# Kernel optimization log

Hardware: AMD Instinct MI355X
Metric: run time of the kernel (lower is better)

The kernel has to match this reference:

```python
import math
import jax, jax.numpy as jnp
import numpy as np

BATCH, DEPTH = 16, 12
N_NODES = 2 ** DEPTH - 1  # 4095, heap layout: children of i are 2i+1, 2i+2
IN_F, OUT_F, STATE_F = 512, 512, 256


def setup_inputs() -> dict:
    key = jax.random.key(0)
    ks = jax.random.split(key, 10)
    x_batch = jax.random.normal(ks[0], (BATCH, N_NODES, IN_F), dtype=jnp.float32)
    idx_batch = jnp.arange(BATCH, dtype=jnp.int32)
    W_in = jax.random.normal(ks[1], (IN_F, IN_F), dtype=jnp.float32) / math.sqrt(IN_F)
    b_in = jnp.zeros((IN_F,), dtype=jnp.float32)
    u1 = jax.random.uniform(ks[2], (STATE_F,), dtype=jnp.float32)
    u2 = jax.random.uniform(ks[3], (STATE_F,), dtype=jnp.float32)
    nu_log = jnp.log(-0.5 * jnp.log(u1 + 1e-6))
    theta_log = jnp.log(2.0 * math.pi * u2)
    lam_mod = jnp.exp(-jnp.exp(nu_log))
    gamma_log = jnp.log(jnp.sqrt(1.0 - jnp.square(lam_mod)))
    B_re = jax.random.normal(ks[4], (STATE_F, IN_F), dtype=jnp.float32) / math.sqrt(2 * IN_F)
    B_im = jax.random.normal(ks[5], (STATE_F, IN_F), dtype=jnp.float32) / math.sqrt(2 * IN_F)
    C_re = jax.random.normal(ks[6], (OUT_F, STATE_F), dtype=jnp.float32) / math.sqrt(STATE_F)
    C_im = jax.random.normal(ks[7], (OUT_F, STATE_F), dtype=jnp.float32) / math.sqrt(STATE_F)
    return dict(x_batch=x_batch, idx_batch=idx_batch, W_in=W_in, b_in=b_in,
                nu_log=nu_log, theta_log=theta_log, gamma_log=gamma_log,
                B_re=B_re, B_im=B_im, C_re=C_re, C_im=C_im)


def reference(x_batch, idx_batch, W_in, b_in, nu_log, theta_log, gamma_log,
              B_re, B_im, C_re, C_im):
    bsz, n_nodes, _ = x_batch.shape
    depth = int(round(math.log2(n_nodes + 1)))
    S = B_re.shape[0]

    # LRU constants (complex lambda kept as (re, im) pair)
    lam_mod = jnp.exp(-jnp.exp(nu_log))           # [S]
    th = jnp.exp(theta_log)
    lr, li = lam_mod * jnp.cos(th), lam_mod * jnp.sin(th)
    gamma = jnp.exp(gamma_log)                    # [S]

    proj = x_batch @ W_in.T + b_in                # [B, N, IN]
    # complex input term (proj is real): proj @ B^T
    in_re = jnp.einsum('bni,si->bns', proj, B_re) # [B, N, S]
    in_im = jnp.einsum('bni,si->bns', proj, B_im)

    h_re = jnp.zeros((bsz, n_nodes, S), dtype=proj.dtype)
    h_im = jnp.zeros((bsz, n_nodes, S), dtype=proj.dtype)

    # process levels bottom-up; level d nodes occupy [2^d-1, 2^{d+1}-1)
    for d in range(depth - 1, -1, -1):
        a, b = 2 ** d - 1, 2 ** (d + 1) - 1
        n = b - a
        if d == depth - 1:  # leaves: left/right = -1 -> zero child state
            cr = jnp.zeros((bsz, n, S), dtype=proj.dtype)
            ci = jnp.zeros((bsz, n, S), dtype=proj.dtype)
        else:
            # children of nodes [a, b) are the contiguous block [2a+1, 2b+1)
            cr = h_re[:, 2 * a + 1:2 * b + 1].reshape(bsz, n, 2, S).sum(axis=2)
            ci = h_im[:, 2 * a + 1:2 * b + 1].reshape(bsz, n, 2, S).sum(axis=2)
        hr = lr * cr - li * ci + gamma * in_re[:, a:b]
        hi = lr * ci + li * cr + gamma * in_im[:, a:b]
        h_re = h_re.at[:, a:b].set(hr)
        h_im = h_im.at[:, a:b].set(hi)

    # y = Re(h @ C^T), computed once on final states (same math as per-level scatter)
    outputs = jnp.einsum('bns,os->bno', h_re, C_re) - jnp.einsum('bns,os->bno', h_im, C_im)
    return outputs
```

## Files before the change

### kernel.cpp

```cpp
#include <hip/hip_runtime.h>


#define ROWS 65520
#define KDIM 512

typedef __attribute__((ext_vector_type(8))) short bf16x8;
typedef __attribute__((ext_vector_type(4))) float f32x4;

__device__ __forceinline__ unsigned short f2bf(float f) {
    unsigned int u = __float_as_uint(f);
    unsigned int r = (u + 0x7FFFu + ((u >> 16) & 1u)) >> 16;
    return (unsigned short)r;
}
__device__ __forceinline__ float b2f(unsigned short h) {
    return __uint_as_float(((unsigned int)h) << 16);
}
__device__ __forceinline__ float b2f_lo(unsigned int p) {
    return __uint_as_float(p << 16);
}
__device__ __forceinline__ float b2f_hi(unsigned int p) {
    return __uint_as_float(p & 0xFFFF0000u);
}

#define PC_BASE   1024
#define PB_BASE   2048
#define CVT_BASE  2176
#define CVT_BLKS  2048
#define PREP_GRID 4224
#define CVT_N4    8386560

__global__ __launch_bounds__(256) void prep_all(const float* __restrict__ x,
                                                unsigned short* __restrict__ x16,
                                                const float* __restrict__ W,
                                                const float* __restrict__ Bre,
                                                const float* __restrict__ Bim,
                                                const float* __restrict__ gamma_log,
                                                unsigned short* __restrict__ M16,
                                                const float* __restrict__ bin,
                                                float* __restrict__ biasc,
                                                const float* __restrict__ Cre,
                                                const float* __restrict__ Cim,
                                                unsigned short* __restrict__ C16) {
    __shared__ float Bs[16][17];
    __shared__ float Ws[16][17];
    const int blk = blockIdx.x;
    const int t = threadIdx.x;

    if (blk < PC_BASE) {
        const int bx = blk & 31;
        const int by = blk >> 5;
        const int tx = t & 15;
        const int ty = t >> 4;
        const int j  = bx * 16 + tx;
        const int cc = by * 16 + ty;
        const float* Bsel = (cc < 256) ? (Bre + (size_t)cc * 512)
                                       : (Bim + (size_t)(cc - 256) * 512);
        float acc = 0.f;
        for (int kt = 0; kt < 512; kt += 16) {
            Bs[ty][tx] = Bsel[kt + tx];
            Ws[ty][tx] = W[(size_t)(kt + ty) * 512 + j];
            __syncthreads();
#pragma unroll
            for (int k = 0; k < 16; ++k) acc += Bs[ty][k] * Ws[k][tx];
            __syncthreads();
        }
        float g = expf(gamma_log[cc & 255]);
        M16[(size_t)cc * 512 + j] = f2bf(acc * g);
    } else if (blk < PB_BASE) {
        int idx = (blk - PC_BASE) * 256 + t;
        int o = idx >> 9;
        int s = idx & 511;
        float v = (s < 256) ? Cre[(size_t)o * 256 + s] : -Cim[(size_t)o * 256 + (s - 256)];
        C16[idx] = f2bf(v);
    } else if (blk < CVT_BASE) {
        const int c = (blk - PB_BASE) * 4 + (t >> 6);
        const int lane = t & 63;
        const float* Bsel = (c < 256) ? (Bre + (size_t)c * 512)
                                      : (Bim + (size_t)(c - 256) * 512);
        float acc = 0.f;
#pragma unroll
        for (int i = lane; i < 512; i += 64) acc += bin[i] * Bsel[i];
#pragma unroll
        for (int off = 32; off > 0; off >>= 1) acc += __shfl_down(acc, off, 64);
        if (lane == 0) biasc[c] = acc * expf(gamma_log[c & 255]);
    } else {
        int i = (blk - CVT_BASE) * 256 + t;
#pragma unroll 4
        for (; i < CVT_N4; i += CVT_BLKS * 256) {
            float4 v = ((const float4*)x)[i];
            ushort4 o;
            o.x = f2bf(v.x); o.y = f2bf(v.y); o.z = f2bf(v.z); o.w = f2bf(v.w);
            ((ushort4*)x16)[i] = o;
        }
    }
}

template <bool OUT_BF16>
__global__ __launch_bounds__(256) void gemm_mfma(const unsigned short* __restrict__ A,
                                                 const unsigned short* __restrict__ Bm,
                                                 const float* __restrict__ bias,
                                                 void* __restrict__ Cout,
                                                 int Mrows) {
    __shared__ __align__(16) unsigned short As[2][128 * 64];
    __shared__ __align__(16) unsigned short Bs[2][128 * 64];
    const int t = threadIdx.x;
    const int lane = t & 63;
    const int w = t >> 6;
    const int wr = (w >> 1) * 64;
    const int wc = (w & 1) * 64;
    const int bid = blockIdx.x;
    const int xcd = bid & 7;
    const int lid = bid >> 3;
    const int rowblk = xcd * 64 + (lid >> 2);
    const int colblk = lid & 3;
    const int row0 = rowblk * 128;
    const int col0 = colblk * 128;
    const int kt0  = (rowblk & 7) * 64;

    f32x4 acc[4][4] = {};

    const unsigned short* gaB[4];
    const unsigned short* gbB[4];
    int ldsoff[4];
#pragma unroll
    for (int q = 0; q < 4; ++q) {
        int c_   = q * 256 + t;
        int row_ = c_ >> 3;
        int kc_  = c_ & 7;
        int kg_  = kc_ ^ (row_ & 7);
        int ar_  = row0 + row_; if (ar_ >= Mrows) ar_ = Mrows - 1;
        gaB[q] = A + (size_t)ar_ * KDIM + kg_ * 8;
        gbB[q] = Bm + (size_t)(col0 + row_) * KDIM + kg_ * 8;
        ldsoff[q] = c_ * 8;
    }

#define STAGE(pb, itv)                                                         \
    do {                                                                       \
        const int kt_ = (kt0 + (itv) * 64) & 511;                              \
        _Pragma("unroll")                                                      \
        for (int q = 0; q < 4; ++q) {                                          \
            __builtin_amdgcn_global_load_lds(                                  \
                (const __attribute__((address_space(1))) unsigned int*)(gaB[q] + kt_),\
                (__attribute__((address_space(3))) unsigned int*)(&As[pb][ldsoff[q]]),\
                16, 0, 0);                                                     \
            __builtin_amdgcn_global_load_lds(                                  \
                (const __attribute__((address_space(1))) unsigned int*)(gbB[q] + kt_),\
                (__attribute__((address_space(3))) unsigned int*)(&Bs[pb][ldsoff[q]]),\
                16, 0, 0);                                                     \
        }                                                                      \
    } while (0)

    STAGE(0, 0);
    __syncthreads();

    int cur = 0;
    for (int it = 0; it < 8; ++it) {
        if (it < 7) STAGE(cur ^ 1, it + 1);
        __builtin_amdgcn_s_setprio(1);
#pragma unroll
        for (int kk = 0; kk < 64; kk += 32) {
            const int kgc = kk >> 3;
            bf16x8 af[4], bfr[4];
#pragma unroll
            for (int i = 0; i < 4; ++i) {
                int row = wr + i * 16 + (lane & 15);
                int kca = (kgc + (lane >> 4)) ^ (row & 7);
                af[i] = *(const bf16x8*)(&As[cur][row * 64 + kca * 8]);
                int colr = wc + i * 16 + (lane & 15);
                int kcb = (kgc + (lane >> 4)) ^ (colr & 7);
                bfr[i] = *(const bf16x8*)(&Bs[cur][colr * 64 + kcb * 8]);
            }
#pragma unroll
            for (int i = 0; i < 4; ++i)
#pragma unroll
                for (int j = 0; j < 4; ++j)
                    acc[i][j] = __builtin_amdgcn_mfma_f32_16x16x32_bf16(
                        af[i], bfr[j], acc[i][j], 0, 0, 0);
        }
        __builtin_amdgcn_s_setprio(0);
        __syncthreads();
        cur ^= 1;
    }
#undef STAGE

    const int cq = lane >> 4;
    const int cl = lane & 15;
#pragma unroll
    for (int i = 0; i < 4; ++i) {
#pragma unroll
        for (int j = 0; j < 4; ++j) {
#pragma unroll
            for (int r = 0; r < 4; ++r) {
                int grow = row0 + wr + i * 16 + cq * 4 + r;
                int gcol = col0 + wc + j * 16 + cl;
                if (grow < Mrows) {
                    float v = acc[i][j][r];
                    if (bias) v += bias[gcol];
                    if (OUT_BF16)
                        ((unsigned short*)Cout)[(size_t)grow * 512 + gcol] = f2bf(v);
                    else
                        ((float*)Cout)[(size_t)grow * 512 + gcol] = v;
                }
            }
        }
    }
}

template <int E>
__global__ __launch_bounds__(256) void tree_up2(unsigned short* __restrict__ buf,
                                                const float* __restrict__ nu_log,
                                                const float* __restrict__ theta_log,
                                                int root_base, int nroots) {
    const int b = blockIdx.x;
    const int h = threadIdx.x >> 7;
    const int j2 = (threadIdx.x & 127) * 2;
    const int rr = blockIdx.y * 2 + h;
    if (rr >= nroots) return;
    const int rs = root_base + rr;
    constexpr int LEAVES = 1 << E;
    constexpr int NODES = LEAVES - 1;

    float lr0, li0, lr1, li1;
    { const float lam = expf(-expf(nu_log[j2]));     const float th = expf(theta_log[j2]);
      lr0 = lam * cosf(th); li0 = lam * sinf(th); }
    { const float lam = expf(-expf(nu_log[j2 + 1])); const float th = expf(theta_log[j2 + 1]);
      lr1 = lam * cosf(th); li1 = lam * sinf(th); }
    const size_t base = (size_t)b * 4095;

    unsigned int pr[LEAVES], pi[LEAVES];
    const int nbL = ((rs + 1) << E) - 1;
#pragma unroll
    for (int i = 0; i < LEAVES; ++i) {
        const size_t r = (base + nbL + i) * 512;
        pr[i] = *(const unsigned int*)(buf + r + j2);
        pi[i] = *(const unsigned int*)(buf + r + 256 + j2);
    }
    unsigned int qr[NODES], qi[NODES];
#pragma unroll
    for (int e = E - 1; e >= 0; --e) {
#pragma unroll
        for (int i = 0; i < (1 << e); ++i) {
            const int idx = LEAVES - (2 << e) + i;
            const size_t r = (base + (((rs + 1) << e) - 1) + i) * 512;
            qr[idx] = *(const unsigned int*)(buf + r + j2);
            qi[idx] = *(const unsigned int*)(buf + r + 256 + j2);
        }
    }
    __builtin_amdgcn_sched_barrier(0);

    float vr0[LEAVES], vi0[LEAVES], vr1[LEAVES], vi1[LEAVES];
#pragma unroll
    for (int i = 0; i < LEAVES; ++i) {
        vr0[i] = b2f_lo(pr[i]); vr1[i] = b2f_hi(pr[i]);
        vi0[i] = b2f_lo(pi[i]); vi1[i] = b2f_hi(pi[i]);
    }
#pragma unroll
    for (int e = E - 1; e >= 0; --e) {
#pragma unroll
        for (int i = 0; i < (1 << e); ++i) {
            const int idx = LEAVES - (2 << e) + i;
            const float cr0 = vr0[2 * i] + vr0[2 * i + 1];
            const float ci0 = vi0[2 * i] + vi0[2 * i + 1];
            const float cr1 = vr1[2 * i] + vr1[2 * i + 1];
            const float ci1 = vi1[2 * i] + vi1[2 * i + 1];
            const float hr0 = lr0 * cr0 - li0 * ci0 + b2f_lo(qr[idx]);
            const float hi0 = lr0 * ci0 + li0 * cr0 + b2f_lo(qi[idx]);
            const float hr1 = lr1 * cr1 - li1 * ci1 + b2f_hi(qr[idx]);
            const float hi1 = lr1 * ci1 + li1 * cr1 + b2f_hi(qi[idx]);
            const size_t r = (base + (((rs + 1) << e) - 1) + i) * 512;
            *(unsigned int*)(buf + r + j2) =
                (unsigned int)f2bf(hr0) | ((unsigned int)f2bf(hr1) << 16);
            *(unsigned int*)(buf + r + 256 + j2) =
                (unsigned int)f2bf(hi0) | ((unsigned int)f2bf(hi1) << 16);
            vr0[i] = hr0; vi0[i] = hi0; vr1[i] = hr1; vi1[i] = hi1;
        }
    }
}

extern "C" void kernel_launch(void* const* d_in, const int* in_sizes, int n_in,
                              void* d_out, int out_size, void* d_ws, size_t ws_size,
                              hipStream_t stream) {
    const float* x         = (const float*)d_in[0];
    const float* W_in      = (const float*)d_in[2];
    const float* b_in      = (const float*)d_in[3];
    const float* nu_log    = (const float*)d_in[4];
    const float* theta_log = (const float*)d_in[5];
    const float* gamma_log = (const float*)d_in[6];
    const float* B_re      = (const float*)d_in[7];
    const float* B_im      = (const float*)d_in[8];
    const float* C_re      = (const float*)d_in[9];
    const float* C_im      = (const float*)d_in[10];
    float* out = (float*)d_out;

    char* ws = (char*)d_ws;
    const size_t HB = (size_t)ROWS * 512 * 2;
    unsigned short* x16   = (unsigned short*)ws;
    unsigned short* hb16  = (unsigned short*)(ws + HB);
    unsigned short* M16   = (unsigned short*)(ws + 2 * HB);
    unsigned short* C16   = (unsigned short*)(ws + 2 * HB + 512 * 512 * 2);
    float*          biasc = (float*)(ws + 2 * HB + 2 * 512 * 512 * 2);

    prep_all<<<PREP_GRID, 256, 0, stream>>>(x, x16, W_in, B_re, B_im, gamma_log,
                                            M16, b_in, biasc, C_re, C_im, C16);

    gemm_mfma<true><<<2048, 256, 0, stream>>>(x16, M16, biasc, hb16, ROWS);

    tree_up2<4><<<dim3(16, 64), 256, 0, stream>>>(hb16, nu_log, theta_log, 127, 128);
    tree_up2<4><<<dim3(16, 4),  256, 0, stream>>>(hb16, nu_log, theta_log, 7, 8);
    tree_up2<3><<<dim3(16, 1),  256, 0, stream>>>(hb16, nu_log, theta_log, 0, 1);

    gemm_mfma<false><<<2048, 256, 0, stream>>>(hb16, C16, nullptr, out, ROWS);
}
```

Before: 399.9 us.

## Replace double-buffered K=64 stages with 4-deep K=32 pipeline and fragment-ordered LDS

Moves the GEMM main loop from two 64-wide K buffers with a full __syncthreads per step to a four-slot ring of 32-wide K tiles, keeping three tiles in flight. Each step uses explicit vmcnt waits and a single barrier. LDS is rearranged so each lane's MFMA fragment sits in a contiguous slot, which removes the XOR swizzle and per-load index math. The per-block K rotation offset is dropped. The risks are more barriers per unit of work, and bank conflicts or unchanged occupancy from the new layout.

Measured after the change: 459.5 us. +14.9%, slower.

```diff
diff --git a/kernel.cpp b/kernel.cpp
--- a/kernel.cpp
+++ b/kernel.cpp
@@ -101,8 +101,8 @@
                                                  const float* __restrict__ bias,
                                                  void* __restrict__ Cout,
                                                  int Mrows) {
-    __shared__ __align__(16) unsigned short As[2][128 * 64];
-    __shared__ __align__(16) unsigned short Bs[2][128 * 64];
+    __shared__ __align__(16) unsigned short As[4 * 4096];
+    __shared__ __align__(16) unsigned short Bs[4 * 4096];
     const int t = threadIdx.x;
     const int lane = t & 63;
     const int w = t >> 6;
@@ -115,72 +115,92 @@
     const int colblk = lid & 3;
     const int row0 = rowblk * 128;
     const int col0 = colblk * 128;
-    const int kt0  = (rowblk & 7) * 64;
 
     f32x4 acc[4][4] = {};
 
-    const unsigned short* gaB[4];
-    const unsigned short* gbB[4];
-    int ldsoff[4];
-#pragma unroll
-    for (int q = 0; q < 4; ++q) {
-        int c_   = q * 256 + t;
-        int row_ = c_ >> 3;
-        int kc_  = c_ & 7;
-        int kg_  = kc_ ^ (row_ & 7);
-        int ar_  = row0 + row_; if (ar_ >= Mrows) ar_ = Mrows - 1;
-        gaB[q] = A + (size_t)ar_ * KDIM + kg_ * 8;
-        gbB[q] = Bm + (size_t)(col0 + row_) * KDIM + kg_ * 8;
-        ldsoff[q] = c_ * 8;
-    }
-
-#define STAGE(pb, itv)                                                         \
+    const unsigned short* gaB[2];
+    const unsigned short* gbB[2];
+    int sl[2];
+#pragma unroll
+    for (int q = 0; q < 2; ++q) {
+        const int s   = q * 256 + t;
+        const int row = ((s >> 5) << 3) + (s & 7);
+        const int kc  = (s >> 3) & 3;
+        int ar = row0 + row; if (ar >= Mrows) ar = Mrows - 1;
+        gaB[q] = A + (size_t)ar * KDIM + kc * 8;
+        gbB[q] = Bm + (size_t)(col0 + row) * KDIM + kc * 8;
+        sl[q] = s;
+    }
+
+    const int l15 = lane & 15;
+    const int aslot = ((wr >> 3) + (l15 >> 3)) * 32 + ((lane >> 4) << 3) + (lane & 7);
+    const int bslot = ((wc >> 3) + (l15 >> 3)) * 32 + ((lane >> 4) << 3) + (lane & 7);
+
+#define STAGE(PB, IT)                                                          \
     do {                                                                       \
-        const int kt_ = (kt0 + (itv) * 64) & 511;                              \
         _Pragma("unroll")                                                      \
-        for (int q = 0; q < 4; ++q) {                                          \
+        for (int q = 0; q < 2; ++q) {                                          \
             __builtin_amdgcn_global_load_lds(                                  \
-                (const __attribute__((address_space(1))) unsigned int*)(gaB[q] + kt_),\
-                (__attribute__((address_space(3))) unsigned int*)(&As[pb][ldsoff[q]]),\
+                (const __attribute__((address_space(1))) unsigned int*)(gaB[q] + (IT) * 32), \
+                (__attribute__((address_space(3))) unsigned int*)(As + (PB) * 4096 + sl[q] * 8), \
                 16, 0, 0);                                                     \
             __builtin_amdgcn_global_load_lds(                                  \
-                (const __attribute__((address_space(1))) unsigned int*)(gbB[q] + kt_),\
-                (__attribute__((address_space(3))) unsigned int*)(&Bs[pb][ldsoff[q]]),\
+                (const __attribute__((address_space(1))) unsigned int*)(gbB[q] + (IT) * 32), \
+                (__attribute__((address_space(3))) unsigned int*)(Bs + (PB) * 4096 + sl[q] * 8), \
                 16, 0, 0);                                                     \
         }                                                                      \
     } while (0)
 
+#define COMPUTE(PB)                                                            \
+    do {                                                                       \
+        bf16x8 af[4], bfr[4];                                                  \
+        _Pragma("unroll")                                                      \
+        for (int i = 0; i < 4; ++i)                                            \
+            af[i] = *(const bf16x8*)(As + (PB) * 4096 + (aslot + i * 64) * 8); \
+        _Pragma("unroll")                                                      \
+        for (int j = 0; j < 4; ++j)                                            \
+            bfr[j] = *(const bf16x8*)(Bs + (PB) * 4096 + (bslot + j * 64) * 8);\
+        _Pragma("unroll")                                                      \
+        for (int i = 0; i < 4; ++i)                                            \
+            _Pragma("unroll")                                                  \
+            for (int j = 0; j < 4; ++j)                                        \
+                acc[i][j] = __builtin_amdgcn_mfma_f32_16x16x32_bf16(           \
+                    af[i], bfr[j], acc[i][j], 0, 0, 0);                        \
+    } while (0)
+
+#define PIPE_ITER(IT, WAITN, DOSTAGE)                                          \
+    do {                                                                       \
+        asm volatile("s_waitcnt vmcnt(" #WAITN ")" ::: "memory");              \
+        __builtin_amdgcn_s_barrier();                                          \
+        if (DOSTAGE) STAGE((IT + 3) & 3, IT + 3);                              \
+        __builtin_amdgcn_s_setprio(1);                                         \
+        COMPUTE((IT) & 3);                                                     \
+        __builtin_amdgcn_s_setprio(0);                                         \
+    } while (0)
+
     STAGE(0, 0);
-    __syncthreads();
-
-    int cur = 0;
-    for (int it = 0; it < 8; ++it) {
-        if (it < 7) STAGE(cur ^ 1, it + 1);
-        __builtin_amdgcn_s_setprio(1);
-#pragma unroll
-        for (int kk = 0; kk < 64; kk += 32) {
-            const int kgc = kk >> 3;
-            bf16x8 af[4], bfr[4];
-#pragma unroll
-            for (int i = 0; i < 4; ++i) {
-                int row = wr + i * 16 + (lane & 15);
-                int kca = (kgc + (lane >> 4)) ^ (row & 7);
-                af[i] = *(const bf16x8*)(&As[cur][row * 64 + kca * 8]);
-                int colr = wc + i * 16 + (lane & 15);
-                int kcb = (kgc + (lane >> 4)) ^ (colr & 7);
-                bfr[i] = *(const bf16x8*)(&Bs[cur][colr * 64 + kcb * 8]);
-            }
-#pragma unroll
-            for (int i = 0; i < 4; ++i)
-#pragma unroll
-                for (int j = 0; j < 4; ++j)
-                    acc[i][j] = __builtin_amdgcn_mfma_f32_16x16x32_bf16(
-                        af[i], bfr[j], acc[i][j], 0, 0, 0);
-        }
-        __builtin_amdgcn_s_setprio(0);
-        __syncthreads();
-        cur ^= 1;
-    }
+    STAGE(1, 1);
+    STAGE(2, 2);
+
+    PIPE_ITER(0, 8, true);
+    PIPE_ITER(1, 8, true);
+    PIPE_ITER(2, 8, true);
+    PIPE_ITER(3, 8, true);
+    PIPE_ITER(4, 8, true);
+    PIPE_ITER(5, 8, true);
+    PIPE_ITER(6, 8, true);
+    PIPE_ITER(7, 8, true);
+    PIPE_ITER(8, 8, true);
+    PIPE_ITER(9, 8, true);
+    PIPE_ITER(10, 8, true);
+    PIPE_ITER(11, 8, true);
+    PIPE_ITER(12, 8, true);
+    PIPE_ITER(13, 8, false);
+    PIPE_ITER(14, 4, false);
+    PIPE_ITER(15, 0, false);
+
+#undef PIPE_ITER
+#undef COMPUTE
 #undef STAGE
 
     const int cq = lane >> 4;
```

## Make GEMM persistent over four row tiles with cross-tile prefetch

Applied to the files above, without the earlier changes.

Each GEMM workgroup now walks four consecutive 128-row tiles instead of one, and the grid shrinks from 2048 to 512 blocks. The A tile for the next row block is prefetched into LDS during the last k-step of the current tile, so the pipeline stays full across tiles and per-block launch and prologue costs are amortised. The trade-off is fewer resident blocks (512 across 256 CUs) and an epilogue store that is not overlapped with the next tile's compute, which can reduce latency hiding and load balance.

New measurement: 398.4 us. About the same (-0.4%).

```diff
diff --git a/kernel.cpp b/kernel.cpp
--- a/kernel.cpp
+++ b/kernel.cpp
@@ -108,102 +108,126 @@
     const int w = t >> 6;
     const int wr = (w >> 1) * 64;
     const int wc = (w & 1) * 64;
-    const int bid = blockIdx.x;
-    const int xcd = bid & 7;
-    const int lid = bid >> 3;
-    const int rowblk = xcd * 64 + (lid >> 2);
-    const int colblk = lid & 3;
-    const int row0 = rowblk * 128;
+    const int p = blockIdx.x;
+    const int xcd = p & 7;
+    const int q = p >> 3;
+    const int colblk = q & 3;
+    const int rg = q >> 2;
     const int col0 = colblk * 128;
-    const int kt0  = (rowblk & 7) * 64;
-
-    f32x4 acc[4][4] = {};
-
-    const unsigned short* gaB[4];
+
+    int arow[4], akoff[4], ldsoff[4];
     const unsigned short* gbB[4];
-    int ldsoff[4];
-#pragma unroll
-    for (int q = 0; q < 4; ++q) {
-        int c_   = q * 256 + t;
+#pragma unroll
+    for (int qq = 0; qq < 4; ++qq) {
+        int c_   = qq * 256 + t;
         int row_ = c_ >> 3;
         int kc_  = c_ & 7;
         int kg_  = kc_ ^ (row_ & 7);
-        int ar_  = row0 + row_; if (ar_ >= Mrows) ar_ = Mrows - 1;
-        gaB[q] = A + (size_t)ar_ * KDIM + kg_ * 8;
-        gbB[q] = Bm + (size_t)(col0 + row_) * KDIM + kg_ * 8;
-        ldsoff[q] = c_ * 8;
-    }
-
-#define STAGE(pb, itv)                                                         \
+        arow[qq]  = row_;
+        akoff[qq] = kg_ * 8;
+        ldsoff[qq] = c_ * 8;
+        gbB[qq] = Bm + (size_t)(col0 + row_) * KDIM + kg_ * 8;
+    }
+    const unsigned short* gaB[4];
+
+#define SET_TILE_A(ROW0)                                                       \
     do {                                                                       \
-        const int kt_ = (kt0 + (itv) * 64) & 511;                              \
         _Pragma("unroll")                                                      \
-        for (int q = 0; q < 4; ++q) {                                          \
+        for (int qq = 0; qq < 4; ++qq) {                                       \
+            int ar_ = (ROW0) + arow[qq]; if (ar_ >= Mrows) ar_ = Mrows - 1;    \
+            gaB[qq] = A + (size_t)ar_ * KDIM + akoff[qq];                      \
+        }                                                                      \
+    } while (0)
+
+#define STAGE(pb, KT)                                                          \
+    do {                                                                       \
+        _Pragma("unroll")                                                      \
+        for (int qq = 0; qq < 4; ++qq) {                                       \
             __builtin_amdgcn_global_load_lds(                                  \
-                (const __attribute__((address_space(1))) unsigned int*)(gaB[q] + kt_),\
-                (__attribute__((address_space(3))) unsigned int*)(&As[pb][ldsoff[q]]),\
+                (const __attribute__((address_space(1))) unsigned int*)(gaB[qq] + (KT)), \
+                (__attribute__((address_space(3))) unsigned int*)(&As[pb][ldsoff[qq]]), \
                 16, 0, 0);                                                     \
             __builtin_amdgcn_global_load_lds(                                  \
-                (const __attribute__((address_space(1))) unsigned int*)(gbB[q] + kt_),\
-                (__attribute__((address_space(3))) unsigned int*)(&Bs[pb][ldsoff[q]]),\
+                (const __attribute__((address_space(1))) unsigned int*)(gbB[qq] + (KT)), \
+                (__attribute__((address_space(3))) unsigned int*)(&Bs[pb][ldsoff[qq]]), \
                 16, 0, 0);                                                     \
         }                                                                      \
     } while (0)
 
-    STAGE(0, 0);
+    f32x4 acc[4][4] = {};
+
+    int rowblk = xcd * 64 + rg * 4;
+    int row0 = rowblk * 128;
+    int kt0 = (rowblk & 7) * 64;
+    SET_TILE_A(row0);
+    STAGE(0, kt0);
     __syncthreads();
 
     int cur = 0;
-    for (int it = 0; it < 8; ++it) {
-        if (it < 7) STAGE(cur ^ 1, it + 1);
-        __builtin_amdgcn_s_setprio(1);
-#pragma unroll
-        for (int kk = 0; kk < 64; kk += 32) {
-            const int kgc = kk >> 3;
-            bf16x8 af[4], bfr[4];
-#pragma unroll
-            for (int i = 0; i < 4; ++i) {
-                int row = wr + i * 16 + (lane & 15);
-                int kca = (kgc + (lane >> 4)) ^ (row & 7);
-                af[i] = *(const bf16x8*)(&As[cur][row * 64 + kca * 8]);
-                int colr = wc + i * 16 + (lane & 15);
-                int kcb = (kgc + (lane >> 4)) ^ (colr & 7);
-                bfr[i] = *(const bf16x8*)(&Bs[cur][colr * 64 + kcb * 8]);
+    for (int j = 0; j < 4; ++j) {
+        for (int it = 0; it < 8; ++it) {
+            if (it < 7) {
+                STAGE(cur ^ 1, (kt0 + (it + 1) * 64) & 511);
+            } else if (j < 3) {
+                const int nrowblk = rowblk + 1;
+                SET_TILE_A(nrowblk * 128);
+                STAGE(cur ^ 1, (nrowblk & 7) * 64);
             }
-#pragma unroll
-            for (int i = 0; i < 4; ++i)
-#pragma unroll
-                for (int j = 0; j < 4; ++j)
-                    acc[i][j] = __builtin_amdgcn_mfma_f32_16x16x32_bf16(
-                        af[i], bfr[j], acc[i][j], 0, 0, 0);
-        }
-        __builtin_amdgcn_s_setprio(0);
-        __syncthreads();
-        cur ^= 1;
-    }
-#undef STAGE
-
-    const int cq = lane >> 4;
-    const int cl = lane & 15;
-#pragma unroll
-    for (int i = 0; i < 4; ++i) {
-#pragma unroll
-        for (int j = 0; j < 4; ++j) {
-#pragma unroll
-            for (int r = 0; r < 4; ++r) {
-                int grow = row0 + wr + i * 16 + cq * 4 + r;
-                int gcol = col0 + wc + j * 16 + cl;
-                if (grow < Mrows) {
-                    float v = acc[i][j][r];
-                    if (bias) v += bias[gcol];
-                    if (OUT_BF16)
-                        ((unsigned short*)Cout)[(size_t)grow * 512 + gcol] = f2bf(v);
-                    else
-                        ((float*)Cout)[(size_t)grow * 512 + gcol] = v;
+            __builtin_amdgcn_s_setprio(1);
+#pragma unroll
+            for (int kk = 0; kk < 64; kk += 32) {
+                const int kgc = kk >> 3;
+                bf16x8 af[4], bfr[4];
+#pragma unroll
+                for (int i = 0; i < 4; ++i) {
+                    int row = wr + i * 16 + (lane & 15);
+                    int kca = (kgc + (lane >> 4)) ^ (row & 7);
+                    af[i] = *(const bf16x8*)(&As[cur][row * 64 + kca * 8]);
+                    int colr = wc + i * 16 + (lane & 15);
+                    int kcb = (kgc + (lane >> 4)) ^ (colr & 7);
+                    bfr[i] = *(const bf16x8*)(&Bs[cur][colr * 64 + kcb * 8]);
+                }
+#pragma unroll
+                for (int i = 0; i < 4; ++i)
+#pragma unroll
+                    for (int jj = 0; jj < 4; ++jj)
+                        acc[i][jj] = __builtin_amdgcn_mfma_f32_16x16x32_bf16(
+                            af[i], bfr[jj], acc[i][jj], 0, 0, 0);
+            }
+            __builtin_amdgcn_s_setprio(0);
+            __syncthreads();
+            cur ^= 1;
+        }
+
+        const int cq = lane >> 4;
+        const int cl = lane & 15;
+#pragma unroll
+        for (int i = 0; i < 4; ++i) {
+#pragma unroll
+            for (int jj = 0; jj < 4; ++jj) {
+#pragma unroll
+                for (int r = 0; r < 4; ++r) {
+                    int grow = row0 + wr + i * 16 + cq * 4 + r;
+                    int gcol = col0 + wc + jj * 16 + cl;
+                    if (grow < Mrows) {
+                        float v = acc[i][jj][r];
+                        if (bias) v += bias[gcol];
+                        if (OUT_BF16)
+                            ((unsigned short*)Cout)[(size_t)grow * 512 + gcol] = f2bf(v);
+                        else
+                            ((float*)Cout)[(size_t)grow * 512 + gcol] = v;
+                    }
+                    acc[i][jj][r] = 0.f;
                 }
             }
         }
-    }
+
+        rowblk += 1;
+        row0 = rowblk * 128;
+        kt0 = (rowblk & 7) * 64;
+    }
+#undef STAGE
+#undef SET_TILE_A
 }
 
 template <int E>
@@ -303,11 +327,11 @@
     prep_all<<<PREP_GRID, 256, 0, stream>>>(x, x16, W_in, B_re, B_im, gamma_log,
                                             M16, b_in, biasc, C_re, C_im, C16);
 
-    gemm_mfma<true><<<2048, 256, 0, stream>>>(x16, M16, biasc, hb16, ROWS);
+    gemm_mfma<true><<<512, 256, 0, stream>>>(x16, M16, biasc, hb16, ROWS);
 
     tree_up2<4><<<dim3(16, 64), 256, 0, stream>>>(hb16, nu_log, theta_log, 127, 128);
     tree_up2<4><<<dim3(16, 4),  256, 0, stream>>>(hb16, nu_log, theta_log, 7, 8);
     tree_up2<3><<<dim3(16, 1),  256, 0, stream>>>(hb16, nu_log, theta_log, 0, 1);
 
-    gemm_mfma<false><<<2048, 256, 0, stream>>>(hb16, C16, nullptr, out, ROWS);
-}
+    gemm_mfma<false><<<512, 256, 0, stream>>>(hb16, C16, nullptr, out, ROWS);
+}
```
